# Kernel optimization log

Measured on AMD Instinct MI355X. Metric: run time of the kernel, lower is better.

## Reference

```python
import jax, jax.numpy as jnp
import numpy as np

N_NODES = 50000
N_EDGES = 800000
D = 128


def gcn_conv(x, W, b, src, dst, num_nodes):
    """PyG GCNConv: x @ W, add self-loops, symmetric normalization, scatter-add, + bias."""
    x = x @ W  # [N, out]
    loop = jnp.arange(num_nodes, dtype=src.dtype)
    s = jnp.concatenate([src, loop])  # [E+N]
    d = jnp.concatenate([dst, loop])
    w = jnp.ones(s.shape[0], x.dtype)  # edge_weight=None -> ones (self-loop fill=1)
    deg = jax.ops.segment_sum(w, d, num_segments=num_nodes)  # [N]
    dinv = jnp.where(deg > 0, jax.lax.rsqrt(deg), 0.0)
    norm = dinv[s] * dinv[d]  # [E+N]
    out = jax.ops.segment_sum(x[s] * norm[:, None], d, num_segments=num_nodes)
    return out + b


def setup_inputs() -> dict:
    key = jax.random.key(0)
    ks = jax.random.split(key, 8)
    sc = 1.0 / np.sqrt(D)
    x = jax.random.normal(ks[0], (N_NODES, D), dtype=jnp.float32)
    edge_index = jax.random.randint(ks[1], (2, N_EDGES), 0, N_NODES)
    W1 = jax.random.normal(ks[2], (D, D), dtype=jnp.float32) * sc
    W2 = jax.random.normal(ks[3], (D, D), dtype=jnp.float32) * sc
    W3 = jax.random.normal(ks[4], (D, D), dtype=jnp.float32) * sc
    b1 = jnp.zeros((D,), jnp.float32)
    b2 = jnp.zeros((D,), jnp.float32)
    b3 = jnp.zeros((D,), jnp.float32)
    return {"x": x, "edge_index": edge_index, "W1": W1, "b1": b1,
            "W2": W2, "b2": b2, "W3": W3, "b3": b3}


def reference(x, edge_index, W1, b1, W2, b2, W3, b3):
    src, dst = edge_index[0], edge_index[1]
    n = x.shape[0]
    x = jax.nn.relu(gcn_conv(x, W1, b1, src, dst, n))
    x = jax.nn.relu(gcn_conv(x, W2, b2, src, dst, n))
    return gcn_conv(x, W3, b3, src, dst, n)
```

## Files before the change

### kernel.cpp

```cpp
#include <hip/hip_runtime.h>
#include <hip/hip_fp16.h>
#include <math.h>

#define D 128

typedef __attribute__((ext_vector_type(8))) _Float16 half8;
typedef __attribute__((ext_vector_type(4))) float f32x4;


__global__ void count_rank_kernel(const int* __restrict__ dst, int* __restrict__ cnt,
                                  int* __restrict__ rank, int E) {
    int e0 = (blockIdx.x * blockDim.x + threadIdx.x) * 4;
    if (e0 + 3 < E) {
        int4 d = *(const int4*)(dst + e0);
        int4 r;
        r.x = atomicAdd(&cnt[d.x], 1);
        r.y = atomicAdd(&cnt[d.y], 1);
        r.z = atomicAdd(&cnt[d.z], 1);
        r.w = atomicAdd(&cnt[d.w], 1);
        *(int4*)(rank + e0) = r;
    } else {
        for (int e = e0; e < E; ++e) rank[e] = atomicAdd(&cnt[dst[e]], 1);
    }
}

__global__ __launch_bounds__(1024) void scan_kernel(const int* __restrict__ cnt,
                                                    int* __restrict__ rowptr,
                                                    float* __restrict__ dinv,
                                                    int N) {
    __shared__ int wsum[16];
    __shared__ int carry_s;
    int tid  = threadIdx.x;
    int lane = tid & 63;
    int wid  = tid >> 6;
    if (tid == 0) carry_s = 0;
    __syncthreads();
    for (int base = 0; base < N; base += 4096) {
        int i = base + tid * 4;
        int4 v = make_int4(0, 0, 0, 0);
        if (i + 3 < N) v = *(const int4*)(cnt + i);
        else {
            if (i + 0 < N) v.x = cnt[i + 0];
            if (i + 1 < N) v.y = cnt[i + 1];
            if (i + 2 < N) v.z = cnt[i + 2];
            if (i + 3 < N) v.w = cnt[i + 3];
        }
        int s0 = v.x, s1 = s0 + v.y, s2 = s1 + v.z, s3 = s2 + v.w;
        int sc = s3;
        #pragma unroll
        for (int off = 1; off < 64; off <<= 1) {
            int t = __shfl_up(sc, off, 64);
            if (lane >= off) sc += t;
        }
        if (lane == 63) wsum[wid] = sc;
        __syncthreads();
        if (tid < 16) {
            int w = wsum[tid];
            #pragma unroll
            for (int off = 1; off < 16; off <<= 1) {
                int t = __shfl_up(w, off, 64);
                if (tid >= off) w += t;
            }
            wsum[tid] = w;
        }
        __syncthreads();
        int waveoff = (wid > 0) ? wsum[wid - 1] : 0;
        int excl = carry_s + waveoff + (sc - s3);
        if (i + 0 < N) { rowptr[i + 0] = excl;      dinv[i + 0] = rsqrtf((float)v.x + 1.0f); }
        if (i + 1 < N) { rowptr[i + 1] = excl + s0; dinv[i + 1] = rsqrtf((float)v.y + 1.0f); }
        if (i + 2 < N) { rowptr[i + 2] = excl + s1; dinv[i + 2] = rsqrtf((float)v.z + 1.0f); }
        if (i + 3 < N) { rowptr[i + 3] = excl + s2; dinv[i + 3] = rsqrtf((float)v.w + 1.0f); }
        __syncthreads();
        if (tid == 0) carry_s += wsum[15];
        __syncthreads();
    }
    if (tid == 0) rowptr[N] = carry_s;
}

__global__ void fill_kernel(const int* __restrict__ src, const int* __restrict__ dst,
                            const int* __restrict__ rank, const int* __restrict__ rowptr,
                            int* __restrict__ col, int E) {
    int e0 = (blockIdx.x * blockDim.x + threadIdx.x) * 4;
    if (e0 + 3 < E) {
        int4 d = *(const int4*)(dst + e0);
        int4 r = *(const int4*)(rank + e0);
        int4 s = *(const int4*)(src + e0);
        int p0 = rowptr[d.x] + r.x;
        int p1 = rowptr[d.y] + r.y;
        int p2 = rowptr[d.z] + r.z;
        int p3 = rowptr[d.w] + r.w;
        col[p0] = s.x;
        col[p1] = s.y;
        col[p2] = s.z;
        col[p3] = s.w;
    } else {
        for (int e = e0; e < E; ++e) col[rowptr[dst[e]] + rank[e]] = src[e];
    }
}


__global__ void convw_kernel(const float* __restrict__ W1, const float* __restrict__ W2,
                             const float* __restrict__ W3, __half* __restrict__ WhT) {
    int i = blockIdx.x * blockDim.x + threadIdx.x;
    int l = i >> 14;
    int j = i & 16383;
    int n = j >> 7, k = j & 127;
    const float* W = (l == 0) ? W1 : (l == 1) ? W2 : W3;
    WhT[(size_t)i] = __float2half(W[(size_t)k * D + n]);
}


__global__ __launch_bounds__(256) void gemm_mfma(const float* __restrict__ X,
                                                 const __half* __restrict__ WhT,
                                                 const float* __restrict__ dinv,
                                                 __half* __restrict__ Y,
                                                 int M, int relu) {
    int tid  = threadIdx.x;
    int wave = tid >> 6;
    int lane = tid & 63;
    int quad = lane >> 4;
    int l16  = lane & 15;
    int m0   = blockIdx.x * 64 + wave * 16;
    if (m0 >= M) return;

    f32x4 acc[8];
    #pragma unroll
    for (int t = 0; t < 8; ++t) acc[t] = (f32x4)0.0f;

    const float* xrow = X + (size_t)(m0 + l16) * D;

    #pragma unroll
    for (int ks = 0; ks < 4; ++ks) {
        int k0 = ks * 32 + quad * 8;
        float4 x0 = *(const float4*)(xrow + k0);
        float4 x1 = *(const float4*)(xrow + k0 + 4);
        if (relu) {
            x0.x = fmaxf(x0.x, 0.f); x0.y = fmaxf(x0.y, 0.f);
            x0.z = fmaxf(x0.z, 0.f); x0.w = fmaxf(x0.w, 0.f);
            x1.x = fmaxf(x1.x, 0.f); x1.y = fmaxf(x1.y, 0.f);
            x1.z = fmaxf(x1.z, 0.f); x1.w = fmaxf(x1.w, 0.f);
        }
        half8 a;
        a[0] = (_Float16)x0.x; a[1] = (_Float16)x0.y;
        a[2] = (_Float16)x0.z; a[3] = (_Float16)x0.w;
        a[4] = (_Float16)x1.x; a[5] = (_Float16)x1.y;
        a[6] = (_Float16)x1.z; a[7] = (_Float16)x1.w;
        #pragma unroll
        for (int t = 0; t < 8; ++t) {
            half8 b = *(const half8*)(WhT + (size_t)(t * 16 + l16) * D + k0);
            acc[t] = __builtin_amdgcn_mfma_f32_16x16x32_f16(a, b, acc[t], 0, 0, 0);
        }
    }

    float4 dv = *(const float4*)(dinv + m0 + quad * 4);
    float dvs[4] = {dv.x, dv.y, dv.z, dv.w};
    #pragma unroll
    for (int t = 0; t < 8; ++t) {
        #pragma unroll
        for (int r = 0; r < 4; ++r) {
            int grow = m0 + quad * 4 + r;
            Y[(size_t)grow * D + t * 16 + l16] = __float2half(acc[t][r] * dvs[r]);
        }
    }
}


__global__ __launch_bounds__(256) void aggregate_kernel(const __half* __restrict__ ys,
                                                        const int* __restrict__ rowptr,
                                                        const int* __restrict__ col,
                                                        const float* __restrict__ dinv,
                                                        const float* __restrict__ b,
                                                        float* __restrict__ out,
                                                        int N) {
    int gwave = (blockIdx.x * blockDim.x + threadIdx.x) >> 6;
    int lane  = threadIdx.x & 63;
    if (gwave >= N) return;
    int row = gwave;
    int s = rowptr[row], e = rowptr[row + 1];

    __half2 hself = ((const __half2*)(ys + (size_t)row * D))[lane];
    float2 a0 = __half22float2(hself);
    float2 a1 = make_float2(0.f, 0.f), a2 = make_float2(0.f, 0.f),
           a3 = make_float2(0.f, 0.f), a4 = make_float2(0.f, 0.f),
           a5 = make_float2(0.f, 0.f), a6 = make_float2(0.f, 0.f),
           a7 = make_float2(0.f, 0.f);

    for (int base = s; base < e; base += 64) {
        int idx = base + lane;
        int myc = (idx < e) ? col[idx] : 0;
        int nb  = min(64, e - base);
        int j = 0;
        for (; j + 8 <= nb; j += 8) {
            int c0 = __shfl(myc, j + 0), c1 = __shfl(myc, j + 1);
            int c2 = __shfl(myc, j + 2), c3 = __shfl(myc, j + 3);
            int c4 = __shfl(myc, j + 4), c5 = __shfl(myc, j + 5);
            int c6 = __shfl(myc, j + 6), c7 = __shfl(myc, j + 7);
            __half2 v0 = ((const __half2*)(ys + (size_t)c0 * D))[lane];
            __half2 v1 = ((const __half2*)(ys + (size_t)c1 * D))[lane];
            __half2 v2 = ((const __half2*)(ys + (size_t)c2 * D))[lane];
            __half2 v3 = ((const __half2*)(ys + (size_t)c3 * D))[lane];
            __half2 v4 = ((const __half2*)(ys + (size_t)c4 * D))[lane];
            __half2 v5 = ((const __half2*)(ys + (size_t)c5 * D))[lane];
            __half2 v6 = ((const __half2*)(ys + (size_t)c6 * D))[lane];
            __half2 v7 = ((const __half2*)(ys + (size_t)c7 * D))[lane];
            a0.x += __low2float(v0); a0.y += __high2float(v0);
            a1.x += __low2float(v1); a1.y += __high2float(v1);
            a2.x += __low2float(v2); a2.y += __high2float(v2);
            a3.x += __low2float(v3); a3.y += __high2float(v3);
            a4.x += __low2float(v4); a4.y += __high2float(v4);
            a5.x += __low2float(v5); a5.y += __high2float(v5);
            a6.x += __low2float(v6); a6.y += __high2float(v6);
            a7.x += __low2float(v7); a7.y += __high2float(v7);
        }
        for (; j < nb; ++j) {
            int c = __shfl(myc, j);
            __half2 v = ((const __half2*)(ys + (size_t)c * D))[lane];
            a0.x += __low2float(v); a0.y += __high2float(v);
        }
    }
    a0.x += a1.x + a2.x + a3.x + a4.x + a5.x + a6.x + a7.x;
    a0.y += a1.y + a2.y + a3.y + a4.y + a5.y + a6.y + a7.y;

    float dv  = dinv[row];
    float2 bb = ((const float2*)b)[lane];
    float2 o  = make_float2(bb.x + dv * a0.x, bb.y + dv * a0.y);
    ((float2*)(out + (size_t)row * D))[lane] = o;
}


extern "C" void kernel_launch(void* const* d_in, const int* in_sizes, int n_in,
                              void* d_out, int out_size, void* d_ws, size_t ws_size,
                              hipStream_t stream) {
    const float* x   = (const float*)d_in[0];
    const int*   ei  = (const int*)d_in[1];
    const float* W1  = (const float*)d_in[2];
    const float* b1  = (const float*)d_in[3];
    const float* W2  = (const float*)d_in[4];
    const float* b2  = (const float*)d_in[5];
    const float* W3  = (const float*)d_in[6];
    const float* b3  = (const float*)d_in[7];
    float* out = (float*)d_out;

    const int N = in_sizes[0] / D;
    const int E = in_sizes[1] / 2;
    const int* src = ei;
    const int* dst = ei + E;

    char* ws = (char*)d_ws;
    size_t off = 0;
    auto alloc = [&](size_t bytes) {
        void* p = ws + off;
        off = (off + bytes + 255) & ~(size_t)255;
        return p;
    };
    __half* ys    = (__half*)alloc((size_t)N * D * sizeof(__half));
    int*   cnt    = (int*)alloc((size_t)N * sizeof(int));
    int*   rowptr = (int*)alloc((size_t)(N + 1) * sizeof(int));
    float* dinv   = (float*)alloc((size_t)N * sizeof(float));
    int*   rank   = (int*)alloc((size_t)E * sizeof(int));
    int*   col    = (int*)alloc((size_t)E * sizeof(int));
    __half* WhT   = (__half*)alloc((size_t)3 * D * D * sizeof(__half));
    (void)ws_size; (void)n_in; (void)out_size;

    convw_kernel<<<(3 * D * D + 255) / 256, 256, 0, stream>>>(W1, W2, W3, WhT);

    hipMemsetAsync(cnt, 0, (size_t)N * sizeof(int), stream);
    count_rank_kernel<<<(E / 4 + 255) / 256, 256, 0, stream>>>(dst, cnt, rank, E);
    scan_kernel<<<1, 1024, 0, stream>>>(cnt, rowptr, dinv, N);
    fill_kernel<<<(E / 4 + 255) / 256, 256, 0, stream>>>(src, dst, rank, rowptr, col, E);

    const int gemm_grid = (N + 63) / 64;
    const int agg_grid  = (N * 64 + 255) / 256;

    gemm_mfma<<<gemm_grid, 256, 0, stream>>>(x, WhT, dinv, ys, N, 0);
    aggregate_kernel<<<agg_grid, 256, 0, stream>>>(ys, rowptr, col, dinv, b1, out, N);
    gemm_mfma<<<gemm_grid, 256, 0, stream>>>(out, WhT + 16384, dinv, ys, N, 1);
    aggregate_kernel<<<agg_grid, 256, 0, stream>>>(ys, rowptr, col, dinv, b2, out, N);
    gemm_mfma<<<gemm_grid, 256, 0, stream>>>(out, WhT + 32768, dinv, ys, N, 1);
    aggregate_kernel<<<agg_grid, 256, 0, stream>>>(ys, rowptr, col, dinv, b3, out, N);
}
```

Before: 341.0 us.

## Store hidden activations in fp16 with fused ReLU and deepen gather unrolling

Intermediate layer outputs are now written as fp16 with ReLU applied inside the aggregation epilogue, and a dedicated fp16-input GEMM reads them directly without converting. This halves the bytes for intermediate writes and GEMM reads. The aggregation gather loop is unrolled to 16 with 8- and 4-wide tails to put more loads in flight. The count and fill CSR kernels now process 8 edges per thread. All of this adds an extra fp16 buffer and rounds activations to half precision between layers.

```diff
diff --git a/kernel.cpp b/kernel.cpp
--- a/kernel.cpp
+++ b/kernel.cpp
@@ -10,15 +10,21 @@
 
 __global__ void count_rank_kernel(const int* __restrict__ dst, int* __restrict__ cnt,
                                   int* __restrict__ rank, int E) {
-    int e0 = (blockIdx.x * blockDim.x + threadIdx.x) * 4;
-    if (e0 + 3 < E) {
-        int4 d = *(const int4*)(dst + e0);
-        int4 r;
-        r.x = atomicAdd(&cnt[d.x], 1);
-        r.y = atomicAdd(&cnt[d.y], 1);
-        r.z = atomicAdd(&cnt[d.z], 1);
-        r.w = atomicAdd(&cnt[d.w], 1);
-        *(int4*)(rank + e0) = r;
+    int e0 = (blockIdx.x * blockDim.x + threadIdx.x) * 8;
+    if (e0 + 7 < E) {
+        int4 da = *(const int4*)(dst + e0);
+        int4 db = *(const int4*)(dst + e0 + 4);
+        int4 ra, rb;
+        ra.x = atomicAdd(&cnt[da.x], 1);
+        ra.y = atomicAdd(&cnt[da.y], 1);
+        ra.z = atomicAdd(&cnt[da.z], 1);
+        ra.w = atomicAdd(&cnt[da.w], 1);
+        rb.x = atomicAdd(&cnt[db.x], 1);
+        rb.y = atomicAdd(&cnt[db.y], 1);
+        rb.z = atomicAdd(&cnt[db.z], 1);
+        rb.w = atomicAdd(&cnt[db.w], 1);
+        *(int4*)(rank + e0)     = ra;
+        *(int4*)(rank + e0 + 4) = rb;
     } else {
         for (int e = e0; e < E; ++e) rank[e] = atomicAdd(&cnt[dst[e]], 1);
     }
@@ -80,19 +86,24 @@
 __global__ void fill_kernel(const int* __restrict__ src, const int* __restrict__ dst,
                             const int* __restrict__ rank, const int* __restrict__ rowptr,
                             int* __restrict__ col, int E) {
-    int e0 = (blockIdx.x * blockDim.x + threadIdx.x) * 4;
-    if (e0 + 3 < E) {
-        int4 d = *(const int4*)(dst + e0);
-        int4 r = *(const int4*)(rank + e0);
-        int4 s = *(const int4*)(src + e0);
-        int p0 = rowptr[d.x] + r.x;
-        int p1 = rowptr[d.y] + r.y;
-        int p2 = rowptr[d.z] + r.z;
-        int p3 = rowptr[d.w] + r.w;
-        col[p0] = s.x;
-        col[p1] = s.y;
-        col[p2] = s.z;
-        col[p3] = s.w;
+    int e0 = (blockIdx.x * blockDim.x + threadIdx.x) * 8;
+    if (e0 + 7 < E) {
+        int4 da = *(const int4*)(dst + e0);
+        int4 db = *(const int4*)(dst + e0 + 4);
+        int4 ra = *(const int4*)(rank + e0);
+        int4 rb = *(const int4*)(rank + e0 + 4);
+        int4 sa = *(const int4*)(src + e0);
+        int4 sb = *(const int4*)(src + e0 + 4);
+        int p0 = rowptr[da.x] + ra.x;
+        int p1 = rowptr[da.y] + ra.y;
+        int p2 = rowptr[da.z] + ra.z;
+        int p3 = rowptr[da.w] + ra.w;
+        int p4 = rowptr[db.x] + rb.x;
+        int p5 = rowptr[db.y] + rb.y;
+        int p6 = rowptr[db.z] + rb.z;
+        int p7 = rowptr[db.w] + rb.w;
+        col[p0] = sa.x; col[p1] = sa.y; col[p2] = sa.z; col[p3] = sa.w;
+        col[p4] = sb.x; col[p5] = sb.y; col[p6] = sb.z; col[p7] = sb.w;
     } else {
         for (int e = e0; e < E; ++e) col[rowptr[dst[e]] + rank[e]] = src[e];
     }
@@ -110,11 +121,10 @@
 }
 
 
-__global__ __launch_bounds__(256) void gemm_mfma(const float* __restrict__ X,
-                                                 const __half* __restrict__ WhT,
-                                                 const float* __restrict__ dinv,
-                                                 __half* __restrict__ Y,
-                                                 int M, int relu) {
+__global__ __launch_bounds__(256) void gemm_mfma_f32(const float* __restrict__ X,
+                                                     const __half* __restrict__ WhT,
+                                                     const float* __restrict__ dinv,
+                                                     __half* __restrict__ Y, int M) {
     int tid  = threadIdx.x;
     int wave = tid >> 6;
     int lane = tid & 63;
@@ -134,12 +144,6 @@
         int k0 = ks * 32 + quad * 8;
         float4 x0 = *(const float4*)(xrow + k0);
         float4 x1 = *(const float4*)(xrow + k0 + 4);
-        if (relu) {
-            x0.x = fmaxf(x0.x, 0.f); x0.y = fmaxf(x0.y, 0.f);
-            x0.z = fmaxf(x0.z, 0.f); x0.w = fmaxf(x0.w, 0.f);
-            x1.x = fmaxf(x1.x, 0.f); x1.y = fmaxf(x1.y, 0.f);
-            x1.z = fmaxf(x1.z, 0.f); x1.w = fmaxf(x1.w, 0.f);
-        }
         half8 a;
         a[0] = (_Float16)x0.x; a[1] = (_Float16)x0.y;
         a[2] = (_Float16)x0.z; a[3] = (_Float16)x0.w;
@@ -164,13 +168,58 @@
     }
 }
 
-
+__global__ __launch_bounds__(256) void gemm_mfma_f16(const __half* __restrict__ Xh,
+                                                     const __half* __restrict__ WhT,
+                                                     const float* __restrict__ dinv,
+                                                     __half* __restrict__ Y, int M) {
+    int tid  = threadIdx.x;
+    int wave = tid >> 6;
+    int lane = tid & 63;
+    int quad = lane >> 4;
+    int l16  = lane & 15;
+    int m0   = blockIdx.x * 64 + wave * 16;
+    if (m0 >= M) return;
+
+    f32x4 acc[8];
+    #pragma unroll
+    for (int t = 0; t < 8; ++t) acc[t] = (f32x4)0.0f;
+
+    const __half* xrow = Xh + (size_t)(m0 + l16) * D;
+
+    #pragma unroll
+    for (int ks = 0; ks < 4; ++ks) {
+        int k0 = ks * 32 + quad * 8;
+        half8 a = *(const half8*)(xrow + k0);
+        #pragma unroll
+        for (int t = 0; t < 8; ++t) {
+            half8 b = *(const half8*)(WhT + (size_t)(t * 16 + l16) * D + k0);
+            acc[t] = __builtin_amdgcn_mfma_f32_16x16x32_f16(a, b, acc[t], 0, 0, 0);
+        }
+    }
+
+    float4 dv = *(const float4*)(dinv + m0 + quad * 4);
+    float dvs[4] = {dv.x, dv.y, dv.z, dv.w};
+    #pragma unroll
+    for (int t = 0; t < 8; ++t) {
+        #pragma unroll
+        for (int r = 0; r < 4; ++r) {
+            int grow = m0 + quad * 4 + r;
+            Y[(size_t)grow * D + t * 16 + l16] = __float2half(acc[t][r] * dvs[r]);
+        }
+    }
+}
+
+
+#define GATHER(vv, cc) __half2 vv = ((const __half2*)(ys + (size_t)(cc) * D))[lane]
+
+template <bool FINAL>
 __global__ __launch_bounds__(256) void aggregate_kernel(const __half* __restrict__ ys,
                                                         const int* __restrict__ rowptr,
                                                         const int* __restrict__ col,
                                                         const float* __restrict__ dinv,
                                                         const float* __restrict__ b,
-                                                        float* __restrict__ out,
+                                                        __half* __restrict__ outh,
+                                                        float* __restrict__ outf,
                                                         int N) {
     int gwave = (blockIdx.x * blockDim.x + threadIdx.x) >> 6;
     int lane  = threadIdx.x & 63;
@@ -190,19 +239,19 @@
         int myc = (idx < e) ? col[idx] : 0;
         int nb  = min(64, e - base);
         int j = 0;
-        for (; j + 8 <= nb; j += 8) {
-            int c0 = __shfl(myc, j + 0), c1 = __shfl(myc, j + 1);
-            int c2 = __shfl(myc, j + 2), c3 = __shfl(myc, j + 3);
-            int c4 = __shfl(myc, j + 4), c5 = __shfl(myc, j + 5);
-            int c6 = __shfl(myc, j + 6), c7 = __shfl(myc, j + 7);
-            __half2 v0 = ((const __half2*)(ys + (size_t)c0 * D))[lane];
-            __half2 v1 = ((const __half2*)(ys + (size_t)c1 * D))[lane];
-            __half2 v2 = ((const __half2*)(ys + (size_t)c2 * D))[lane];
-            __half2 v3 = ((const __half2*)(ys + (size_t)c3 * D))[lane];
-            __half2 v4 = ((const __half2*)(ys + (size_t)c4 * D))[lane];
-            __half2 v5 = ((const __half2*)(ys + (size_t)c5 * D))[lane];
-            __half2 v6 = ((const __half2*)(ys + (size_t)c6 * D))[lane];
-            __half2 v7 = ((const __half2*)(ys + (size_t)c7 * D))[lane];
+        for (; j + 16 <= nb; j += 16) {
+            int c0 = __shfl(myc, j + 0),  c1 = __shfl(myc, j + 1);
+            int c2 = __shfl(myc, j + 2),  c3 = __shfl(myc, j + 3);
+            int c4 = __shfl(myc, j + 4),  c5 = __shfl(myc, j + 5);
+            int c6 = __shfl(myc, j + 6),  c7 = __shfl(myc, j + 7);
+            int c8 = __shfl(myc, j + 8),  c9 = __shfl(myc, j + 9);
+            int cA = __shfl(myc, j + 10), cB = __shfl(myc, j + 11);
+            int cC = __shfl(myc, j + 12), cD = __shfl(myc, j + 13);
+            int cE = __shfl(myc, j + 14), cF = __shfl(myc, j + 15);
+            GATHER(v0, c0); GATHER(v1, c1); GATHER(v2, c2); GATHER(v3, c3);
+            GATHER(v4, c4); GATHER(v5, c5); GATHER(v6, c6); GATHER(v7, c7);
+            GATHER(v8, c8); GATHER(v9, c9); GATHER(vA, cA); GATHER(vB, cB);
+            GATHER(vC, cC); GATHER(vD, cD); GATHER(vE, cE); GATHER(vF, cF);
             a0.x += __low2float(v0); a0.y += __high2float(v0);
             a1.x += __low2float(v1); a1.y += __high2float(v1);
             a2.x += __low2float(v2); a2.y += __high2float(v2);
@@ -211,10 +260,43 @@
             a5.x += __low2float(v5); a5.y += __high2float(v5);
             a6.x += __low2float(v6); a6.y += __high2float(v6);
             a7.x += __low2float(v7); a7.y += __high2float(v7);
+            a0.x += __low2float(v8); a0.y += __high2float(v8);
+            a1.x += __low2float(v9); a1.y += __high2float(v9);
+            a2.x += __low2float(vA); a2.y += __high2float(vA);
+            a3.x += __low2float(vB); a3.y += __high2float(vB);
+            a4.x += __low2float(vC); a4.y += __high2float(vC);
+            a5.x += __low2float(vD); a5.y += __high2float(vD);
+            a6.x += __low2float(vE); a6.y += __high2float(vE);
+            a7.x += __low2float(vF); a7.y += __high2float(vF);
+        }
+        for (; j + 8 <= nb; j += 8) {
+            int c0 = __shfl(myc, j + 0), c1 = __shfl(myc, j + 1);
+            int c2 = __shfl(myc, j + 2), c3 = __shfl(myc, j + 3);
+            int c4 = __shfl(myc, j + 4), c5 = __shfl(myc, j + 5);
+            int c6 = __shfl(myc, j + 6), c7 = __shfl(myc, j + 7);
+            GATHER(v0, c0); GATHER(v1, c1); GATHER(v2, c2); GATHER(v3, c3);
+            GATHER(v4, c4); GATHER(v5, c5); GATHER(v6, c6); GATHER(v7, c7);
+            a0.x += __low2float(v0); a0.y += __high2float(v0);
+            a1.x += __low2float(v1); a1.y += __high2float(v1);
+            a2.x += __low2float(v2); a2.y += __high2float(v2);
+            a3.x += __low2float(v3); a3.y += __high2float(v3);
+            a4.x += __low2float(v4); a4.y += __high2float(v4);
+            a5.x += __low2float(v5); a5.y += __high2float(v5);
+            a6.x += __low2float(v6); a6.y += __high2float(v6);
+            a7.x += __low2float(v7); a7.y += __high2float(v7);
+        }
+        for (; j + 4 <= nb; j += 4) {
+            int c0 = __shfl(myc, j + 0), c1 = __shfl(myc, j + 1);
+            int c2 = __shfl(myc, j + 2), c3 = __shfl(myc, j + 3);
+            GATHER(v0, c0); GATHER(v1, c1); GATHER(v2, c2); GATHER(v3, c3);
+            a0.x += __low2float(v0); a0.y += __high2float(v0);
+            a1.x += __low2float(v1); a1.y += __high2float(v1);
+            a2.x += __low2float(v2); a2.y += __high2float(v2);
+            a3.x += __low2float(v3); a3.y += __high2float(v3);
         }
         for (; j < nb; ++j) {
             int c = __shfl(myc, j);
-            __half2 v = ((const __half2*)(ys + (size_t)c * D))[lane];
+            GATHER(v, c);
             a0.x += __low2float(v); a0.y += __high2float(v);
         }
     }
@@ -223,8 +305,14 @@
 
     float dv  = dinv[row];
     float2 bb = ((const float2*)b)[lane];
-    float2 o  = make_float2(bb.x + dv * a0.x, bb.y + dv * a0.y);
-    ((float2*)(out + (size_t)row * D))[lane] = o;
+    float rx = bb.x + dv * a0.x;
+    float ry = bb.y + dv * a0.y;
+    if (FINAL) {
+        ((float2*)(outf + (size_t)row * D))[lane] = make_float2(rx, ry);
+    } else {
+        __half2 hv = __floats2half2_rn(fmaxf(rx, 0.f), fmaxf(ry, 0.f));
+        ((__half2*)(outh + (size_t)row * D))[lane] = hv;
+    }
 }
 
 
@@ -254,6 +342,7 @@
         return p;
     };
     __half* ys    = (__half*)alloc((size_t)N * D * sizeof(__half));
+    __half* hs    = (__half*)alloc((size_t)N * D * sizeof(__half));
     int*   cnt    = (int*)alloc((size_t)N * sizeof(int));
     int*   rowptr = (int*)alloc((size_t)(N + 1) * sizeof(int));
     float* dinv   = (float*)alloc((size_t)N * sizeof(float));
@@ -265,17 +354,18 @@
     convw_kernel<<<(3 * D * D + 255) / 256, 256, 0, stream>>>(W1, W2, W3, WhT);
 
     hipMemsetAsync(cnt, 0, (size_t)N * sizeof(int), stream);
-    count_rank_kernel<<<(E / 4 + 255) / 256, 256, 0, stream>>>(dst, cnt, rank, E);
+    const int egrid = ((E + 7) / 8 + 255) / 256;
+    count_rank_kernel<<<egrid, 256, 0, stream>>>(dst, cnt, rank, E);
     scan_kernel<<<1, 1024, 0, stream>>>(cnt, rowptr, dinv, N);
-    fill_kernel<<<(E / 4 + 255) / 256, 256, 0, stream>>>(src, dst, rank, rowptr, col, E);
+    fill_kernel<<<egrid, 256, 0, stream>>>(src, dst, rank, rowptr, col, E);
 
     const int gemm_grid = (N + 63) / 64;
     const int agg_grid  = (N * 64 + 255) / 256;
 
-    gemm_mfma<<<gemm_grid, 256, 0, stream>>>(x, WhT, dinv, ys, N, 0);
-    aggregate_kernel<<<agg_grid, 256, 0, stream>>>(ys, rowptr, col, dinv, b1, out, N);
-    gemm_mfma<<<gemm_grid, 256, 0, stream>>>(out, WhT + 16384, dinv, ys, N, 1);
-    aggregate_kernel<<<agg_grid, 256, 0, stream>>>(ys, rowptr, col, dinv, b2, out, N);
-    gemm_mfma<<<gemm_grid, 256, 0, stream>>>(out, WhT + 32768, dinv, ys, N, 1);
-    aggregate_kernel<<<agg_grid, 256, 0, stream>>>(ys, rowptr, col, dinv, b3, out, N);
-}
+    gemm_mfma_f32<<<gemm_grid, 256, 0, stream>>>(x, WhT, dinv, ys, N);
+    aggregate_kernel<false><<<agg_grid, 256, 0, stream>>>(ys, rowptr, col, dinv, b1, hs, nullptr, N);
+    gemm_mfma_f16<<<gemm_grid, 256, 0, stream>>>(hs, WhT + 16384, dinv, ys, N);
+    aggregate_kernel<false><<<agg_grid, 256, 0, stream>>>(ys, rowptr, col, dinv, b2, hs, nullptr, N);
+    gemm_mfma_f16<<<gemm_grid, 256, 0, stream>>>(hs, WhT + 32768, dinv, ys, N);
+    aggregate_kernel<true><<<agg_grid, 256, 0, stream>>>(ys, rowptr, col, dinv, b3, nullptr, out, N);
+}
```

Measured after the change: 334.5 us. Within noise of the previous version (-1.9%).
